# Optimization experiments

Measured on AMD Instinct MI355X. Metric: run time of the kernel, lower is better.

Reference implementation:

```python
import jax, jax.numpy as jnp
import numpy as np

B = 4096
V_ECC, V_ERR = 16, 12
T = 25
C_T = 32            # temporal_out
F_IN = C_T * T      # 800 = ChebConv in_channels
GCN_OUT = 64
HID2 = 256          # hidden_size * 2


def _ring_edge_index(n):
    # undirected ring (both directions), no self loops -- AHA-segment-style adjacency
    s = np.arange(n); t = (s + 1) % n
    return np.stack([np.concatenate([s, t]), np.concatenate([t, s])]).astype(np.int64)


def setup_inputs() -> dict:
    key = jax.random.key(0)
    ks = iter(jax.random.split(key, 24))
    p = lambda shape, sc=0.05: jax.random.normal(next(ks), shape, jnp.float32) * sc
    return {
        "ecc": jax.random.normal(next(ks), (B, V_ECC, T), jnp.float32),
        "err": jax.random.normal(next(ks), (B, V_ERR, T), jnp.float32),
        "conv_ecc_w": p((C_T, 1, 3)), "conv_ecc_b": p((C_T,)),
        "conv_err_w": p((C_T, 1, 3)), "conv_err_b": p((C_T,)),
        "cheb_ecc_W": p((2, F_IN, GCN_OUT)), "cheb_ecc_b": p((GCN_OUT,)),
        "cheb_err_W": p((2, F_IN, GCN_OUT)), "cheb_err_b": p((GCN_OUT,)),
        "ecc_proj_W": p((V_ECC * GCN_OUT, HID2)), "ecc_proj_b": p((HID2,)),
        "err_proj_W": p((V_ERR * GCN_OUT, HID2)), "err_proj_b": p((HID2,)),
        "attn_W": p((HID2, 1)), "attn_b": p((1,)),
        "fc2_W": p((HID2, 1)), "fc2_b": p((1,)),
        "edge_index_ecc": jnp.asarray(_ring_edge_index(V_ECC)),
        "edge_index_err": jnp.asarray(_ring_edge_index(V_ERR)),
    }


def _temporal_conv(x, w, b):
    # torch Conv1d(1, C_T, kernel=3, padding=1) applied per node, then
    # reshape(B, V, C_T*T) exactly like the torch code (channel-major per node).
    Bv, V, T_ = x.shape
    y = jax.lax.conv_general_dilated(x.reshape(Bv * V, 1, T_), w, (1,), [(1, 1)],
                                     dimension_numbers=("NCH", "OIH", "NCH"))
    y = y + b[None, :, None]
    return y.reshape(Bv, V, -1)  # [B, V, C_T*T]


def _cheb_conv(x, edge_index, W, b):
    # PyG ChebConv(K=2, normalization='sym', lambda_max=2.0):
    #   Lhat = 2 L / lambda_max - I = -D^{-1/2} A D^{-1/2}
    #   out  = Tx0 @ W[0] + Tx1 @ W[1] + b,  Tx0 = x, Tx1 = Lhat x
    # Batched over B with a single segment_sum (replaces the per-sample loop).
    src, dst = edge_index[0], edge_index[1]
    V = x.shape[1]
    deg = jax.ops.segment_sum(jnp.ones(src.shape, jnp.float32), src, num_segments=V)
    dis = jnp.where(deg > 0, jax.lax.rsqrt(jnp.maximum(deg, 1.0)), 0.0)
    w_e = -dis[src] * dis[dst]                        # [E]
    msg = x[:, src, :] * w_e[None, :, None]           # [B, E, F] gather
    Tx1 = jax.ops.segment_sum(msg.transpose(1, 0, 2), dst, num_segments=V)  # [V, B, F]
    Tx1 = Tx1.transpose(1, 0, 2)                      # [B, V, F] scatter-add
    return jnp.einsum("bvf,fo->bvo", x, W[0]) + jnp.einsum("bvf,fo->bvo", Tx1, W[1]) + b


def reference(ecc, err, conv_ecc_w, conv_ecc_b, conv_err_w, conv_err_b,
              cheb_ecc_W, cheb_ecc_b, cheb_err_W, cheb_err_b,
              ecc_proj_W, ecc_proj_b, err_proj_W, err_proj_b,
              attn_W, attn_b, fc2_W, fc2_b, edge_index_ecc, edge_index_err):
    Bv = ecc.shape[0]
    ecc_f = _temporal_conv(ecc, conv_ecc_w, conv_ecc_b)   # [B, 16, 800]
    err_f = _temporal_conv(err, conv_err_w, conv_err_b)   # [B, 12, 800]
    ecc_out = _cheb_conv(ecc_f, edge_index_ecc, cheb_ecc_W, cheb_ecc_b)  # [B, 16, 64]
    err_out = _cheb_conv(err_f, edge_index_err, cheb_err_W, cheb_err_b)  # [B, 12, 64]
    # gated fusion
    ecc_g = ecc_out.reshape(Bv, -1) @ ecc_proj_W + ecc_proj_b  # [B, 256]
    err_g = err_out.reshape(Bv, -1) @ err_proj_W + err_proj_b  # [B, 256]
    attn = jax.nn.sigmoid(jnp.tanh(ecc_g + err_g) @ attn_W + attn_b)  # [B, 1]
    fused = attn * ecc_g + (1.0 - attn) * err_g   # latent_layer (gated path skips fc1)
    x = jax.nn.relu(fused) @ fc2_W + fc2_b        # dropout = identity (eval mode)
    return jax.nn.sigmoid(x)                      # [B, 1]
```

## Files before the change

### kernel.cpp

```cpp
#include <hip/hip_runtime.h>
#include <hip/hip_bf16.h>
#include <math.h>


#define TM 16
#define HID2 256
#define KE 400
#define KR 300
#define CE 13
#define CR 10

#define OFF_A0   6400
#define OFF_B0   6656
#define KBF_ECC  7040
#define KBF_ERR  60288

typedef __attribute__((ext_vector_type(8))) short  short8;
typedef __attribute__((ext_vector_type(4))) float  f32x4;

static __device__ __forceinline__ float ldv(const void* p, int i, bool f32) {
    return f32 ? ((const float*)p)[i]
               : __bfloat162float(((const __hip_bfloat16*)p)[i]);
}

static __device__ __forceinline__ bool detect_f32(const void* ecc) {
    unsigned w = ((const unsigned*)ecc)[threadIdx.x & 63];
    int e0 = (w >> 7) & 0xff, e1 = (w >> 23) & 0xff;
    return __any((e0 >= 141) || (e1 >= 141)) != 0;
}

static __device__ __forceinline__ int bswz(int k, int o) {
    int c = k >> 5, q = (k >> 3) & 3, j = k & 7;
    int nt = o >> 4, li = o & 15;
    return (c * 16 + nt) * 512 + (q * 16 + li) * 8 + j;
}

static __device__ __forceinline__ unsigned pack_bf16(float x0, float x1) {
    __hip_bfloat16 h0 = __float2bfloat16(x0), h1 = __float2bfloat16(x1);
    unsigned u0 = *(unsigned short*)&h0, u1 = *(unsigned short*)&h1;
    return (u1 << 16) | u0;
}

__global__ __launch_bounds__(512) void precompute(
        const void* __restrict__ ecc,
        const void* __restrict__ conv_ecc_w, const void* __restrict__ conv_err_w,
        const void* __restrict__ conv_ecc_b, const void* __restrict__ conv_err_b,
        const void* __restrict__ cheb_ecc_W, const void* __restrict__ cheb_err_W,
        const void* __restrict__ cheb_ecc_b, const void* __restrict__ cheb_err_b,
        const void* __restrict__ ecc_proj_W, const void* __restrict__ err_proj_W,
        const void* __restrict__ ecc_proj_b, const void* __restrict__ err_proj_b,
        float* __restrict__ ws) {
    bool f32 = detect_f32(ecc);
    int tid = threadIdx.x;
    unsigned short* KbE = (unsigned short*)(ws + KBF_ECC);
    unsigned short* KbR = (unsigned short*)(ws + KBF_ERR);
    __shared__ float s0[512], s1[512], w0_s[64], w1_s[64], part[512];

    if (blockIdx.x < 700) {
        int row = blockIdx.x;
        int sig = (row >= KE);
        int lr  = sig ? row - KE : row;
        int v = lr / 25, tp = lr % 25;
        int V = sig ? 12 : 16;
        const void* cw = sig ? conv_err_w : conv_ecc_w;
        const void* W  = sig ? cheb_err_W : cheb_ecc_W;
        const void* P  = sig ? err_proj_W : ecc_proj_W;

        {
            int j = tid & 63, cq = tid >> 6;
            float a0 = 0.f, a1 = 0.f;
            #pragma unroll
            for (int cc = 0; cc < 4; ++cc) {
                int c = cq * 4 + cc;
                #pragma unroll
                for (int k = 0; k < 3; ++k) {
                    int t = tp + 1 - k;
                    if (t >= 0 && t < 25) {
                        float cwv = ldv(cw, c * 3 + k, f32);
                        a0 += cwv * ldv(W, (c * 25 + t) * 64 + j, f32);
                        a1 += cwv * ldv(W, 800 * 64 + (c * 25 + t) * 64 + j, f32);
                    }
                }
            }
            s0[tid] = a0; s1[tid] = a1;
            __syncthreads();
            if (tid < 64) {
                float v0 = 0.f, v1 = 0.f;
                #pragma unroll
                for (int g = 0; g < 8; ++g) { v0 += s0[tid + 64 * g]; v1 += s1[tid + 64 * g]; }
                w0_s[tid] = v0; w1_s[tid] = v1;
            }
            __syncthreads();
        }
        int o = tid & 255, jh = tid >> 8;
        int vp = (v + 1) % V, vm = (v + V - 1) % V;
        float acc = 0.f, sacc = 0.f;
        #pragma unroll 4
        for (int jj = 0; jj < 32; ++jj) {
            int j = jh * 32 + jj;
            acc  += w0_s[j] * ldv(P, (v  * 64 + j) * HID2 + o, f32);
            sacc += w1_s[j] * (ldv(P, (vp * 64 + j) * HID2 + o, f32)
                             + ldv(P, (vm * 64 + j) * HID2 + o, f32));
        }
        part[tid] = acc - 0.5f * sacc;
        __syncthreads();
        if (jh == 0) {
            float kval = part[o] + part[o + 256];
            __hip_bfloat16 h = __float2bfloat16(kval);
            (sig ? KbR : KbE)[bswz(lr, o)] = *(unsigned short*)&h;
        }
    } else if (blockIdx.x < 702) {
        int sig = blockIdx.x - 700;
        int V = sig ? 12 : 16;
        const void* convb = sig ? conv_err_b : conv_ecc_b;
        const void* W     = sig ? cheb_err_W : cheb_ecc_W;
        const void* chebb = sig ? cheb_err_b : cheb_ecc_b;
        const void* P     = sig ? err_proj_W : ecc_proj_W;
        const void* pb    = sig ? err_proj_b : ecc_proj_b;

        {
            int j = tid & 63, g = tid >> 6;
            float acc = 0.f;
            for (int q = 0; q < 100; ++q) {
                int p = g * 100 + q, c = p / 25, t = p % 25;
                acc += ldv(convb, c, f32)
                     * (ldv(W, (c * 25 + t) * 64 + j, f32)
                      - ldv(W, 800 * 64 + (c * 25 + t) * 64 + j, f32));
            }
            s0[tid] = acc;
            __syncthreads();
            if (tid < 64) {
                float v0 = 0.f;
                #pragma unroll
                for (int gg = 0; gg < 8; ++gg) v0 += s0[tid + 64 * gg];
                w0_s[tid] = v0 + ldv(chebb, tid, f32);
            }
            __syncthreads();
        }
        int o = tid & 255, jh = tid >> 8;
        float acc = 0.f;
        for (int v = 0; v < V; ++v)
            #pragma unroll 4
            for (int jj = 0; jj < 32; ++jj) {
                int j = jh * 32 + jj;
                acc += w0_s[j] * ldv(P, (v * 64 + j) * HID2 + o, f32);
            }
        part[tid] = acc;
        __syncthreads();
        if (jh == 0)
            ws[(sig ? OFF_B0 : OFF_A0) + o] = part[o] + part[o + 256] + ldv(pb, o, f32);
    } else {
        for (int idx = tid; idx < (16 + 20) * 256; idx += 512) {
            if (idx < 16 * 256) KbE[bswz(400 + (idx >> 8), idx & 255)] = 0;
            else {
                int i2 = idx - 16 * 256;
                KbR[bswz(300 + (i2 >> 8), i2 & 255)] = 0;
            }
        }
    }
}

#define XR_DW 3328

__global__ __launch_bounds__(512, 2) void main_gemm(
        const void* __restrict__ ecc, const void* __restrict__ err,
        const void* __restrict__ attn_W, const void* __restrict__ attn_b,
        const void* __restrict__ fc2_W, const void* __restrict__ fc2_b,
        const float* __restrict__ ws, void* __restrict__ out) {
    __shared__ float smem[2 * 16 * 257];
    unsigned* xs = (unsigned*)smem;

    bool f32 = detect_f32(ecc);
    int tid  = threadIdx.x;
    int row0 = blockIdx.x * TM;

    if (!f32) {
        const uint4* pe4 = (const uint4*)ecc;
        for (int idx = tid; idx < 16 * 50; idx += 512) {
            int r = idx / 50, i4 = idx - r * 50, i2 = 4 * i4;
            uint4 u = pe4[(row0 + r) * 50 + i4];
            *(uint4*)(xs + (i2 >> 4) * 256 + r * 16 + (i2 & 15)) = u;
        }
        if (tid < 32) {
            int r = tid >> 1, i2 = 200 + (tid & 1) * 4;
            *(uint4*)(xs + (i2 >> 4) * 256 + r * 16 + (i2 & 15)) = make_uint4(0, 0, 0, 0);
        }
        const uint2* pr2 = (const uint2*)err;
        for (int idx = tid; idx < 16 * 75; idx += 512) {
            int r = idx / 75, ip = idx - r * 75, i2 = 2 * ip;
            uint2 u = pr2[(row0 + r) * 75 + ip];
            *(uint2*)(xs + XR_DW + (i2 >> 4) * 256 + r * 16 + (i2 & 15)) = u;
        }
        if (tid < 80) {
            int r = tid / 5, i2 = 150 + (tid % 5) * 2;
            *(uint2*)(xs + XR_DW + (i2 >> 4) * 256 + r * 16 + (i2 & 15)) = make_uint2(0, 0);
        }
    } else {
        for (int idx = tid; idx < 16 * 208; idx += 512) {
            int r = idx / 208, i2 = idx - r * 208;
            unsigned u = 0;
            if (i2 < 200)
                u = pack_bf16(((const float*)ecc)[(row0 + r) * 400 + 2 * i2],
                              ((const float*)ecc)[(row0 + r) * 400 + 2 * i2 + 1]);
            xs[(i2 >> 4) * 256 + r * 16 + (i2 & 15)] = u;
        }
        for (int idx = tid; idx < 16 * 160; idx += 512) {
            int r = idx / 160, i2 = idx - r * 160;
            unsigned u = 0;
            if (i2 < 150)
                u = pack_bf16(((const float*)err)[(row0 + r) * 300 + 2 * i2],
                              ((const float*)err)[(row0 + r) * 300 + 2 * i2 + 1]);
            xs[XR_DW + (i2 >> 4) * 256 + r * 16 + (i2 & 15)] = u;
        }
    }
    __syncthreads();

    int wv = tid >> 6, lane = tid & 63;
    int m = lane & 15, quad = lane >> 4;
    int nt0 = wv * 2;

    const short8* KbE = (const short8*)(ws + KBF_ECC);
    const short8* KbR = (const short8*)(ws + KBF_ERR);
    const char* abase = (const char*)smem + m * 64 + quad * 16;

    f32x4 acc_e[2] = {{0.f, 0.f, 0.f, 0.f}, {0.f, 0.f, 0.f, 0.f}};
    f32x4 acc_r[2] = {{0.f, 0.f, 0.f, 0.f}, {0.f, 0.f, 0.f, 0.f}};

    #pragma unroll
    for (int c = 0; c < CE; ++c) {
        short8 a = *(const short8*)(abase + c * 1024);
        #pragma unroll
        for (int t = 0; t < 2; ++t)
            acc_e[t] = __builtin_amdgcn_mfma_f32_16x16x32_bf16(
                a, KbE[(c * 16 + nt0 + t) * 64 + lane], acc_e[t], 0, 0, 0);
    }
    #pragma unroll
    for (int c = 0; c < CR; ++c) {
        short8 a = *(const short8*)(abase + XR_DW * 4 + c * 1024);
        #pragma unroll
        for (int t = 0; t < 2; ++t)
            acc_r[t] = __builtin_amdgcn_mfma_f32_16x16x32_bf16(
                a, KbR[(c * 16 + nt0 + t) * 64 + lane], acc_r[t], 0, 0, 0);
    }
    __syncthreads();

    float* ge_s = smem;
    float* gr_s = smem + 16 * 257;
    #pragma unroll
    for (int t = 0; t < 2; ++t) {
        int col = (nt0 + t) * 16 + m;
        float a0v = ws[OFF_A0 + col], b0v = ws[OFF_B0 + col];
        #pragma unroll
        for (int i = 0; i < 4; ++i) {
            int row = quad * 4 + i;
            ge_s[row * 257 + col] = acc_e[t][i] + a0v;
            gr_s[row * 257 + col] = acc_r[t][i] + b0v;
        }
    }
    __syncthreads();

    float aw[4], fw[4];
    #pragma unroll
    for (int j = 0; j < 4; ++j) {
        aw[j] = ldv(attn_W, lane + 64 * j, f32);
        fw[j] = ldv(fc2_W,  lane + 64 * j, f32);
    }
    float ab = ldv(attn_b, 0, f32), fb = ldv(fc2_b, 0, f32);
    #pragma unroll
    for (int rr = 0; rr < 2; ++rr) {
        int r = wv * 2 + rr;
        float ge[4], gr[4];
        #pragma unroll
        for (int j = 0; j < 4; ++j) {
            ge[j] = ge_s[r * 257 + lane + 64 * j];
            gr[j] = gr_s[r * 257 + lane + 64 * j];
        }
        float p = 0.f;
        #pragma unroll
        for (int j = 0; j < 4; ++j) p += tanhf(ge[j] + gr[j]) * aw[j];
        #pragma unroll
        for (int off = 32; off; off >>= 1) p += __shfl_down(p, off);
        float a = 1.f / (1.f + expf(-(__shfl(p, 0) + ab)));
        float p2 = 0.f;
        #pragma unroll
        for (int j = 0; j < 4; ++j) {
            float fu = a * ge[j] + (1.f - a) * gr[j];
            p2 += fmaxf(fu, 0.f) * fw[j];
        }
        #pragma unroll
        for (int off = 32; off; off >>= 1) p2 += __shfl_down(p2, off);
        if (lane == 0) {
            float vout = 1.f / (1.f + expf(-(p2 + fb)));
            if (f32) ((float*)out)[row0 + r] = vout;
            else     ((__hip_bfloat16*)out)[row0 + r] = __float2bfloat16(vout);
        }
    }
}

extern "C" void kernel_launch(void* const* d_in, const int* in_sizes, int n_in,
                              void* d_out, int out_size, void* d_ws, size_t ws_size,
                              hipStream_t stream) {
    const void* ecc        = d_in[0];
    const void* err        = d_in[1];
    const void* conv_ecc_w = d_in[2];
    const void* conv_ecc_b = d_in[3];
    const void* conv_err_w = d_in[4];
    const void* conv_err_b = d_in[5];
    const void* cheb_ecc_W = d_in[6];
    const void* cheb_ecc_b = d_in[7];
    const void* cheb_err_W = d_in[8];
    const void* cheb_err_b = d_in[9];
    const void* ecc_proj_W = d_in[10];
    const void* ecc_proj_b = d_in[11];
    const void* err_proj_W = d_in[12];
    const void* err_proj_b = d_in[13];
    const void* attn_W     = d_in[14];
    const void* attn_b     = d_in[15];
    const void* fc2_W      = d_in[16];
    const void* fc2_b      = d_in[17];
    float* ws = (float*)d_ws;

    precompute<<<703, 512, 0, stream>>>(ecc, conv_ecc_w, conv_err_w, conv_ecc_b,
                                        conv_err_b, cheb_ecc_W, cheb_err_W,
                                        cheb_ecc_b, cheb_err_b, ecc_proj_W,
                                        err_proj_W, ecc_proj_b, err_proj_b, ws);
    main_gemm<<<4096 / TM, 512, 0, stream>>>(ecc, err, attn_W, attn_b, fc2_W, fc2_b,
                                             ws, d_out);
}
```

Before: 157.4 us.

## Split weight precompute into two kernels and reuse proj loads across timesteps

The single 703-block precompute kernel is split in two. The first kernel computes the conv-folded Chebyshev weights once per timestep and stores them in the workspace, instead of recomputing them in every (node, timestep) block. The second kernel processes 5 timesteps per block, so each projection weight load serves five accumulators, cutting redundant global reads by about 5x. The cost is an extra kernel launch with a workspace round-trip dependency, and fewer blocks in the second stage, which may underfill the GPU.

```diff
diff --git a/kernel.cpp b/kernel.cpp
--- a/kernel.cpp
+++ b/kernel.cpp
@@ -12,6 +12,7 @@
 
 #define OFF_A0   6400
 #define OFF_B0   6656
+#define OFF_CV   6912
 #define KBF_ECC  7040
 #define KBF_ERR  60288
 
@@ -41,12 +42,61 @@
     return (u1 << 16) | u0;
 }
 
-__global__ __launch_bounds__(512) void precompute(
+__global__ __launch_bounds__(256) void precompute1(
         const void* __restrict__ ecc,
         const void* __restrict__ conv_ecc_w, const void* __restrict__ conv_err_w,
         const void* __restrict__ conv_ecc_b, const void* __restrict__ conv_err_b,
         const void* __restrict__ cheb_ecc_W, const void* __restrict__ cheb_err_W,
         const void* __restrict__ cheb_ecc_b, const void* __restrict__ cheb_err_b,
+        float* __restrict__ ws) {
+    bool f32 = detect_f32(ecc);
+    int tid = threadIdx.x, j = tid & 63, g = tid >> 6;
+    __shared__ float s[256];
+    if (blockIdx.x < 100) {
+        int m = blockIdx.x / 25, tp = blockIdx.x % 25;
+        const void* cw = (m < 2) ? conv_ecc_w : conv_err_w;
+        const void* W  = (m < 2) ? cheb_ecc_W : cheb_err_W;
+        int wofs = (m & 1) * (800 * 64);
+        float acc = 0.f;
+        #pragma unroll
+        for (int cc = 0; cc < 8; ++cc) {
+            int c = g * 8 + cc;
+            #pragma unroll
+            for (int k = 0; k < 3; ++k) {
+                int t = tp + 1 - k;
+                if (t >= 0 && t < 25)
+                    acc += ldv(cw, c * 3 + k, f32) * ldv(W, wofs + (c * 25 + t) * 64 + j, f32);
+            }
+        }
+        s[tid] = acc;
+        __syncthreads();
+        if (tid < 64)
+            ws[m * 1600 + tp * 64 + j] = s[tid] + s[tid + 64] + s[tid + 128] + s[tid + 192];
+    } else {
+        int sig = blockIdx.x - 100;
+        const void* convb = sig ? conv_err_b : conv_ecc_b;
+        const void* W     = sig ? cheb_err_W : cheb_ecc_W;
+        const void* chebb = sig ? cheb_err_b : cheb_ecc_b;
+        float acc = 0.f;
+        #pragma unroll
+        for (int cc = 0; cc < 8; ++cc) {
+            int c = g * 8 + cc;
+            float bc = ldv(convb, c, f32);
+            #pragma unroll 5
+            for (int t = 0; t < 25; ++t)
+                acc += bc * (ldv(W, (c * 25 + t) * 64 + j, f32)
+                           - ldv(W, 800 * 64 + (c * 25 + t) * 64 + j, f32));
+        }
+        s[tid] = acc;
+        __syncthreads();
+        if (tid < 64)
+            ws[OFF_CV + sig * 64 + j] =
+                s[tid] + s[tid + 64] + s[tid + 128] + s[tid + 192] + ldv(chebb, tid, f32);
+    }
+}
+
+__global__ __launch_bounds__(512) void precompute2(
+        const void* __restrict__ ecc,
         const void* __restrict__ ecc_proj_W, const void* __restrict__ err_proj_W,
         const void* __restrict__ ecc_proj_b, const void* __restrict__ err_proj_b,
         float* __restrict__ ws) {
@@ -54,109 +104,73 @@
     int tid = threadIdx.x;
     unsigned short* KbE = (unsigned short*)(ws + KBF_ECC);
     unsigned short* KbR = (unsigned short*)(ws + KBF_ERR);
-    __shared__ float s0[512], s1[512], w0_s[64], w1_s[64], part[512];
-
-    if (blockIdx.x < 700) {
-        int row = blockIdx.x;
-        int sig = (row >= KE);
-        int lr  = sig ? row - KE : row;
-        int v = lr / 25, tp = lr % 25;
+    __shared__ float w0_s[5 * 64], w1_s[5 * 64], part[5 * 512];
+
+    if (blockIdx.x < 140) {
+        int b = blockIdx.x;
+        int sig = (b >= 80);
+        int lb  = sig ? b - 80 : b;
+        int v = lb / 5, tp0 = (lb % 5) * 5;
         int V = sig ? 12 : 16;
-        const void* cw = sig ? conv_err_w : conv_ecc_w;
-        const void* W  = sig ? cheb_err_W : cheb_ecc_W;
-        const void* P  = sig ? err_proj_W : ecc_proj_W;
-
-        {
-            int j = tid & 63, cq = tid >> 6;
-            float a0 = 0.f, a1 = 0.f;
-            #pragma unroll
-            for (int cc = 0; cc < 4; ++cc) {
-                int c = cq * 4 + cc;
-                #pragma unroll
-                for (int k = 0; k < 3; ++k) {
-                    int t = tp + 1 - k;
-                    if (t >= 0 && t < 25) {
-                        float cwv = ldv(cw, c * 3 + k, f32);
-                        a0 += cwv * ldv(W, (c * 25 + t) * 64 + j, f32);
-                        a1 += cwv * ldv(W, 800 * 64 + (c * 25 + t) * 64 + j, f32);
-                    }
-                }
-            }
-            s0[tid] = a0; s1[tid] = a1;
-            __syncthreads();
-            if (tid < 64) {
-                float v0 = 0.f, v1 = 0.f;
-                #pragma unroll
-                for (int g = 0; g < 8; ++g) { v0 += s0[tid + 64 * g]; v1 += s1[tid + 64 * g]; }
-                w0_s[tid] = v0; w1_s[tid] = v1;
-            }
-            __syncthreads();
-        }
+        const void* P = sig ? err_proj_W : ecc_proj_W;
+        const float* W0 = ws + (sig ? 3200 : 0)    + tp0 * 64;
+        const float* W1 = ws + (sig ? 4800 : 1600) + tp0 * 64;
+        if (tid < 320) { w0_s[tid] = W0[tid]; w1_s[tid] = W1[tid]; }
+        __syncthreads();
+
         int o = tid & 255, jh = tid >> 8;
         int vp = (v + 1) % V, vm = (v + V - 1) % V;
-        float acc = 0.f, sacc = 0.f;
-        #pragma unroll 4
+        float acc[5] = {0.f, 0.f, 0.f, 0.f, 0.f};
+        #pragma unroll 8
         for (int jj = 0; jj < 32; ++jj) {
             int j = jh * 32 + jj;
-            acc  += w0_s[j] * ldv(P, (v  * 64 + j) * HID2 + o, f32);
-            sacc += w1_s[j] * (ldv(P, (vp * 64 + j) * HID2 + o, f32)
-                             + ldv(P, (vm * 64 + j) * HID2 + o, f32));
-        }
-        part[tid] = acc - 0.5f * sacc;
+            float p0  = ldv(P, (v  * 64 + j) * HID2 + o, f32);
+            float p1m = -0.5f * (ldv(P, (vp * 64 + j) * HID2 + o, f32)
+                               + ldv(P, (vm * 64 + j) * HID2 + o, f32));
+            #pragma unroll
+            for (int i = 0; i < 5; ++i)
+                acc[i] = fmaf(w0_s[i * 64 + j], p0,
+                         fmaf(w1_s[i * 64 + j], p1m, acc[i]));
+        }
+        #pragma unroll
+        for (int i = 0; i < 5; ++i) part[i * 512 + tid] = acc[i];
         __syncthreads();
         if (jh == 0) {
-            float kval = part[o] + part[o + 256];
-            __hip_bfloat16 h = __float2bfloat16(kval);
-            (sig ? KbR : KbE)[bswz(lr, o)] = *(unsigned short*)&h;
-        }
-    } else if (blockIdx.x < 702) {
-        int sig = blockIdx.x - 700;
+            #pragma unroll
+            for (int i = 0; i < 5; ++i) {
+                float kval = part[i * 512 + o] + part[i * 512 + 256 + o];
+                __hip_bfloat16 h = __float2bfloat16(kval);
+                (sig ? KbR : KbE)[bswz(v * 25 + tp0 + i, o)] = *(unsigned short*)&h;
+            }
+        }
+    } else {
+        int sig = blockIdx.x - 140;
         int V = sig ? 12 : 16;
-        const void* convb = sig ? conv_err_b : conv_ecc_b;
-        const void* W     = sig ? cheb_err_W : cheb_ecc_W;
-        const void* chebb = sig ? cheb_err_b : cheb_ecc_b;
-        const void* P     = sig ? err_proj_W : ecc_proj_W;
-        const void* pb    = sig ? err_proj_b : ecc_proj_b;
-
-        {
-            int j = tid & 63, g = tid >> 6;
-            float acc = 0.f;
-            for (int q = 0; q < 100; ++q) {
-                int p = g * 100 + q, c = p / 25, t = p % 25;
-                acc += ldv(convb, c, f32)
-                     * (ldv(W, (c * 25 + t) * 64 + j, f32)
-                      - ldv(W, 800 * 64 + (c * 25 + t) * 64 + j, f32));
-            }
-            s0[tid] = acc;
-            __syncthreads();
-            if (tid < 64) {
-                float v0 = 0.f;
-                #pragma unroll
-                for (int gg = 0; gg < 8; ++gg) v0 += s0[tid + 64 * gg];
-                w0_s[tid] = v0 + ldv(chebb, tid, f32);
-            }
-            __syncthreads();
-        }
+        const void* P  = sig ? err_proj_W : ecc_proj_W;
+        const void* pb = sig ? err_proj_b : ecc_proj_b;
+        if (sig == 0) {
+            for (int idx = tid; idx < 16 * 256; idx += 512)
+                KbE[bswz(400 + (idx >> 8), idx & 255)] = 0;
+        } else {
+            for (int idx = tid; idx < 20 * 256; idx += 512)
+                KbR[bswz(300 + (idx >> 8), idx & 255)] = 0;
+        }
+        __shared__ float cv_s[64];
+        if (tid < 64) cv_s[tid] = ws[OFF_CV + sig * 64 + tid];
+        __syncthreads();
         int o = tid & 255, jh = tid >> 8;
         float acc = 0.f;
-        for (int v = 0; v < V; ++v)
-            #pragma unroll 4
+        for (int v = 0; v < V; ++v) {
+            #pragma unroll 8
             for (int jj = 0; jj < 32; ++jj) {
                 int j = jh * 32 + jj;
-                acc += w0_s[j] * ldv(P, (v * 64 + j) * HID2 + o, f32);
+                acc += cv_s[j] * ldv(P, (v * 64 + j) * HID2 + o, f32);
             }
+        }
         part[tid] = acc;
         __syncthreads();
         if (jh == 0)
-            ws[(sig ? OFF_B0 : OFF_A0) + o] = part[o] + part[o + 256] + ldv(pb, o, f32);
-    } else {
-        for (int idx = tid; idx < (16 + 20) * 256; idx += 512) {
-            if (idx < 16 * 256) KbE[bswz(400 + (idx >> 8), idx & 255)] = 0;
-            else {
-                int i2 = idx - 16 * 256;
-                KbR[bswz(300 + (i2 >> 8), i2 & 255)] = 0;
-            }
-        }
+            ws[(sig ? OFF_B0 : OFF_A0) + o] = part[o] + part[256 + o] + ldv(pb, o, f32);
     }
 }
 
@@ -320,10 +334,11 @@
     const void* fc2_b      = d_in[17];
     float* ws = (float*)d_ws;
 
-    precompute<<<703, 512, 0, stream>>>(ecc, conv_ecc_w, conv_err_w, conv_ecc_b,
-                                        conv_err_b, cheb_ecc_W, cheb_err_W,
-                                        cheb_ecc_b, cheb_err_b, ecc_proj_W,
-                                        err_proj_W, ecc_proj_b, err_proj_b, ws);
+    precompute1<<<102, 256, 0, stream>>>(ecc, conv_ecc_w, conv_err_w, conv_ecc_b,
+                                         conv_err_b, cheb_ecc_W, cheb_err_W,
+                                         cheb_ecc_b, cheb_err_b, ws);
+    precompute2<<<142, 512, 0, stream>>>(ecc, ecc_proj_W, err_proj_W,
+                                         ecc_proj_b, err_proj_b, ws);
     main_gemm<<<4096 / TM, 512, 0, stream>>>(ecc, err, attn_W, attn_b, fc2_W, fc2_b,
                                              ws, d_out);
 }
```

New measurement: 160.1 us. No clear change (+1.8%).

## Process five temporal rows per precompute block to reuse projection weight loads

Applied to the files above, without the earlier changes.

The precompute kernel now has each block handle five consecutive time positions of one node instead of one row. Each loaded projection-weight element therefore feeds five accumulators, which cuts the redundant global reads of P by about five times and shrinks the grid from 703 to 142 blocks. The padding-zeroing work is folded into the two bias blocks, and the Chebyshev reduction over channels now runs serially per thread rather than split across eight groups. The trade-off is fewer blocks for the GPU to spread across, more work per thread, and more shared memory per block.

```diff
diff --git a/kernel.cpp b/kernel.cpp
--- a/kernel.cpp
+++ b/kernel.cpp
@@ -54,63 +54,64 @@
     int tid = threadIdx.x;
     unsigned short* KbE = (unsigned short*)(ws + KBF_ECC);
     unsigned short* KbR = (unsigned short*)(ws + KBF_ERR);
-    __shared__ float s0[512], s1[512], w0_s[64], w1_s[64], part[512];
-
-    if (blockIdx.x < 700) {
-        int row = blockIdx.x;
-        int sig = (row >= KE);
-        int lr  = sig ? row - KE : row;
-        int v = lr / 25, tp = lr % 25;
+    __shared__ float w0_s[5 * 64], w1_s[5 * 64], part[5 * 512];
+
+    if (blockIdx.x < 140) {
+        int b = blockIdx.x;
+        int sig = (b >= 80);
+        int lb  = sig ? b - 80 : b;
+        int v = lb / 5, tp0 = (lb % 5) * 5;
         int V = sig ? 12 : 16;
         const void* cw = sig ? conv_err_w : conv_ecc_w;
         const void* W  = sig ? cheb_err_W : cheb_ecc_W;
         const void* P  = sig ? err_proj_W : ecc_proj_W;
 
-        {
-            int j = tid & 63, cq = tid >> 6;
+        if (tid < 320) {
+            int i = tid >> 6, j = tid & 63, tb = tp0 + i;
             float a0 = 0.f, a1 = 0.f;
-            #pragma unroll
-            for (int cc = 0; cc < 4; ++cc) {
-                int c = cq * 4 + cc;
+            #pragma unroll 4
+            for (int c = 0; c < 32; ++c) {
                 #pragma unroll
                 for (int k = 0; k < 3; ++k) {
-                    int t = tp + 1 - k;
+                    int t = tb + 1 - k;
                     if (t >= 0 && t < 25) {
                         float cwv = ldv(cw, c * 3 + k, f32);
                         a0 += cwv * ldv(W, (c * 25 + t) * 64 + j, f32);
-                        a1 += cwv * ldv(W, 800 * 64 + (c * 25 + t) * 64 + j, f32);
+                        a1 += cwv * ldv(W, 51200 + (c * 25 + t) * 64 + j, f32);
                     }
                 }
             }
-            s0[tid] = a0; s1[tid] = a1;
-            __syncthreads();
-            if (tid < 64) {
-                float v0 = 0.f, v1 = 0.f;
-                #pragma unroll
-                for (int g = 0; g < 8; ++g) { v0 += s0[tid + 64 * g]; v1 += s1[tid + 64 * g]; }
-                w0_s[tid] = v0; w1_s[tid] = v1;
-            }
-            __syncthreads();
-        }
+            w0_s[tid] = a0; w1_s[tid] = a1;
+        }
+        __syncthreads();
+
         int o = tid & 255, jh = tid >> 8;
         int vp = (v + 1) % V, vm = (v + V - 1) % V;
-        float acc = 0.f, sacc = 0.f;
-        #pragma unroll 4
+        float acc[5] = {0.f, 0.f, 0.f, 0.f, 0.f};
+        #pragma unroll 8
         for (int jj = 0; jj < 32; ++jj) {
             int j = jh * 32 + jj;
-            acc  += w0_s[j] * ldv(P, (v  * 64 + j) * HID2 + o, f32);
-            sacc += w1_s[j] * (ldv(P, (vp * 64 + j) * HID2 + o, f32)
-                             + ldv(P, (vm * 64 + j) * HID2 + o, f32));
-        }
-        part[tid] = acc - 0.5f * sacc;
+            float p0  = ldv(P, (v  * 64 + j) * HID2 + o, f32);
+            float p1m = -0.5f * (ldv(P, (vp * 64 + j) * HID2 + o, f32)
+                               + ldv(P, (vm * 64 + j) * HID2 + o, f32));
+            #pragma unroll
+            for (int i = 0; i < 5; ++i)
+                acc[i] = fmaf(w0_s[i * 64 + j], p0,
+                         fmaf(w1_s[i * 64 + j], p1m, acc[i]));
+        }
+        #pragma unroll
+        for (int i = 0; i < 5; ++i) part[i * 512 + tid] = acc[i];
         __syncthreads();
         if (jh == 0) {
-            float kval = part[o] + part[o + 256];
-            __hip_bfloat16 h = __float2bfloat16(kval);
-            (sig ? KbR : KbE)[bswz(lr, o)] = *(unsigned short*)&h;
-        }
-    } else if (blockIdx.x < 702) {
-        int sig = blockIdx.x - 700;
+            #pragma unroll
+            for (int i = 0; i < 5; ++i) {
+                float kval = part[i * 512 + o] + part[i * 512 + 256 + o];
+                __hip_bfloat16 h = __float2bfloat16(kval);
+                (sig ? KbR : KbE)[bswz(v * 25 + tp0 + i, o)] = *(unsigned short*)&h;
+            }
+        }
+    } else {
+        int sig = blockIdx.x - 140;
         int V = sig ? 12 : 16;
         const void* convb = sig ? conv_err_b : conv_ecc_b;
         const void* W     = sig ? cheb_err_W : cheb_ecc_W;
@@ -118,14 +119,24 @@
         const void* P     = sig ? err_proj_W : ecc_proj_W;
         const void* pb    = sig ? err_proj_b : ecc_proj_b;
 
+        if (sig == 0) {
+            for (int idx = tid; idx < 16 * 256; idx += 512)
+                KbE[bswz(400 + (idx >> 8), idx & 255)] = 0;
+        } else {
+            for (int idx = tid; idx < 20 * 256; idx += 512)
+                KbR[bswz(300 + (idx >> 8), idx & 255)] = 0;
+        }
+
+        __shared__ float s0[512], cv_s[64];
         {
             int j = tid & 63, g = tid >> 6;
             float acc = 0.f;
+            #pragma unroll 4
             for (int q = 0; q < 100; ++q) {
                 int p = g * 100 + q, c = p / 25, t = p % 25;
                 acc += ldv(convb, c, f32)
                      * (ldv(W, (c * 25 + t) * 64 + j, f32)
-                      - ldv(W, 800 * 64 + (c * 25 + t) * 64 + j, f32));
+                      - ldv(W, 51200 + (c * 25 + t) * 64 + j, f32));
             }
             s0[tid] = acc;
             __syncthreads();
@@ -133,30 +144,23 @@
                 float v0 = 0.f;
                 #pragma unroll
                 for (int gg = 0; gg < 8; ++gg) v0 += s0[tid + 64 * gg];
-                w0_s[tid] = v0 + ldv(chebb, tid, f32);
+                cv_s[tid] = v0 + ldv(chebb, tid, f32);
             }
             __syncthreads();
         }
         int o = tid & 255, jh = tid >> 8;
         float acc = 0.f;
-        for (int v = 0; v < V; ++v)
-            #pragma unroll 4
+        for (int v = 0; v < V; ++v) {
+            #pragma unroll 8
             for (int jj = 0; jj < 32; ++jj) {
                 int j = jh * 32 + jj;
-                acc += w0_s[j] * ldv(P, (v * 64 + j) * HID2 + o, f32);
-            }
+                acc += cv_s[j] * ldv(P, (v * 64 + j) * HID2 + o, f32);
+            }
+        }
         part[tid] = acc;
         __syncthreads();
         if (jh == 0)
-            ws[(sig ? OFF_B0 : OFF_A0) + o] = part[o] + part[o + 256] + ldv(pb, o, f32);
-    } else {
-        for (int idx = tid; idx < (16 + 20) * 256; idx += 512) {
-            if (idx < 16 * 256) KbE[bswz(400 + (idx >> 8), idx & 255)] = 0;
-            else {
-                int i2 = idx - 16 * 256;
-                KbR[bswz(300 + (i2 >> 8), i2 & 255)] = 0;
-            }
-        }
+            ws[(sig ? OFF_B0 : OFF_A0) + o] = part[o] + part[256 + o] + ldv(pb, o, f32);
     }
 }
 
@@ -320,7 +324,7 @@
     const void* fc2_b      = d_in[17];
     float* ws = (float*)d_ws;
 
-    precompute<<<703, 512, 0, stream>>>(ecc, conv_ecc_w, conv_err_w, conv_ecc_b,
+    precompute<<<142, 512, 0, stream>>>(ecc, conv_ecc_w, conv_err_w, conv_ecc_b,
                                         conv_err_b, cheb_ecc_W, cheb_err_W,
                                         cheb_ecc_b, cheb_err_b, ecc_proj_W,
                                         err_proj_W, ecc_proj_b, err_proj_b, ws);
```

New measurement: 151.7 us. 1.04x faster.
